# Performance work log

Measured on AMD Instinct MI355X. Metric: run time of the kernel, lower is better.

## Reference

```python
import jax, jax.numpy as jnp
import numpy as np

BATCH, TIMESTEPS, DIM, OUT = 64, 512, 1024, 1024


def setup_inputs() -> dict:
    key = jax.random.key(0)
    k1, k2, k3, k4, k5, k6 = jax.random.split(key, 6)
    # glorot-normal-ish scales for params
    def glorot(k, shape):
        fan_in, fan_out = shape[0], shape[-1]
        std = (2.0 / (fan_in + fan_out)) ** 0.5
        return jax.random.normal(k, shape, dtype=jnp.float32) * std
    return {
        "inputs": jax.random.normal(k1, (BATCH, TIMESTEPS, DIM), dtype=jnp.float32),
        "prev_state": jax.random.normal(k2, (BATCH, OUT), dtype=jnp.float32),
        "Wa": glorot(k3, (OUT, OUT)),
        "Ua": glorot(k4, (DIM, OUT)),
        "Va": glorot(k5, (OUT, 1)),
        "Ba": glorot(k6, (1, OUT)),
    }


def reference(inputs, prev_state, Wa, Ua, Va, Ba):
    # WaS: [B, 1, OUT] broadcast over timesteps
    WaS = jnp.einsum("bo,op->bp", prev_state, Wa)[:, None, :]
    # UaH: [B, T, OUT]
    UaH = jnp.einsum("btd,do->bto", inputs, Ua)
    scores = jnp.tanh(UaH + WaS + Ba)            # [B, T, OUT]
    scores = jax.nn.relu(scores @ Va)            # [B, T, 1]
    sm = jax.nn.softmax(scores, axis=1)          # softmax over timesteps
    context_vector = jnp.sum(inputs * sm, axis=1)  # [B, DIM]
    return context_vector
```

## Files before the change

kernel.cpp:

```cpp
#include <hip/hip_runtime.h>


typedef _Float16 h8 __attribute__((ext_vector_type(8)));
typedef _Float16 h4 __attribute__((ext_vector_type(4)));
typedef float f16v __attribute__((ext_vector_type(16)));

__device__ __forceinline__ float tanh_fast(float x) {
    float e = __expf(2.0f * x);
    return 1.0f - 2.0f * __builtin_amdgcn_rcpf(e + 1.0f);
}

__global__ __launch_bounds__(256) void k_pack_ua(const float* __restrict__ Ua,
                                                 _Float16* __restrict__ B16) {
    int t = blockIdx.x * 256 + threadIdx.x;
    int nn = t & 31, kg = (t >> 5) & 1, ks = (t >> 6) & 63, nt = t >> 12;
    int n = (nt << 5) + nn;
    int kbase = (ks << 4) + (kg << 3);
    h8 v;
#pragma unroll
    for (int j = 0; j < 8; ++j) v[j] = (_Float16)Ua[(size_t)(kbase + j) * 1024 + n];
    *(h8*)(B16 + ((size_t)t << 3)) = v;
}

__global__ __launch_bounds__(256) void k_was_part(const float* __restrict__ ps,
                                                  const float* __restrict__ Wa,
                                                  float* __restrict__ part) {
    int ic = blockIdx.x >> 2, psl = blockIdx.x & 3;
    int tid = threadIdx.x, wv = tid >> 6, lane = tid & 63;
    int p4 = psl * 64 + lane;
    const float4* Wa4 = (const float4*)Wa;
    float4* part4 = (float4*)part;
#pragma unroll 1
    for (int c = 0; c < 4; ++c) {
        int o0 = ic * 128 + c * 32;
        float4 w[32];
#pragma unroll
        for (int o = 0; o < 32; ++o) w[o] = Wa4[(size_t)(o0 + o) * 256 + p4];
#pragma unroll 1
        for (int bb = 0; bb < 16; ++bb) {
            int b = wv * 16 + bb;
            const float* psb = ps + b * 1024 + o0;
            size_t oidx = (size_t)((ic << 6) + b) * 256 + p4;
            float4 a;
            if (c == 0) { a.x = a.y = a.z = a.w = 0.f; }
            else        { a = part4[oidx]; }
#pragma unroll
            for (int o = 0; o < 32; ++o) {
                float s = psb[o];
                a.x += s * w[o].x; a.y += s * w[o].y;
                a.z += s * w[o].z; a.w += s * w[o].w;
            }
            part4[oidx] = a;
        }
    }
}

__global__ __launch_bounds__(256) void k_was_reduce(const float* __restrict__ part,
                                                    const float* __restrict__ Ba,
                                                    float* __restrict__ wsWaS) {
    int b = blockIdx.x, tid = threadIdx.x;
    const float4* p4 = (const float4*)part;
    float4 acc = ((const float4*)Ba)[tid];
#pragma unroll
    for (int ic = 0; ic < 8; ++ic) {
        float4 v = p4[((ic << 6) + b) * 256 + tid];
        acc.x += v.x; acc.y += v.y; acc.z += v.z; acc.w += v.w;
    }
    ((float4*)wsWaS)[b * 256 + tid] = acc;
}

#define AST 136
__global__ __launch_bounds__(256, 1) void k_fused_gemm(
    const float* __restrict__ inputs, const _Float16* __restrict__ B16,
    const float* __restrict__ wsWaS, const float* __restrict__ Va,
    float* __restrict__ scores)
{
    __shared__ _Float16 Ash[2][128 * AST];
    __shared__ float scoreSh[128];
    const int tid = threadIdx.x;
    const int lane = tid & 63, wv = tid >> 6;
    const int l31 = lane & 31, lhi = lane >> 5;
    const int r0 = blockIdx.x * 128;
    const int b = r0 >> 9;
    const int srow = tid >> 1, sq = tid & 1;
    const float4* srcBase = (const float4*)inputs + (size_t)(r0 + srow) * 256 + sq * 16;

    if (tid < 128) scoreSh[tid] = 0.0f;

    for (int pass = 0; pass < 2; ++pass) {
        const int ntb = (pass << 4) + (wv << 2);
        f16v acc[4][4];
#pragma unroll
        for (int rt = 0; rt < 4; ++rt)
#pragma unroll
            for (int ct = 0; ct < 4; ++ct)
#pragma unroll
                for (int e = 0; e < 16; ++e) acc[rt][ct][e] = 0.0f;

        float4 vA[16];
#pragma unroll
        for (int j = 0; j < 16; ++j) vA[j] = srcBase[j];
        {
            _Float16* dst = &Ash[0][srow * AST + sq * 64];
#pragma unroll
            for (int j = 0; j < 8; ++j) {
                float4 v0 = vA[2 * j], v1 = vA[2 * j + 1];
                *(h8*)(dst + j * 8) = (h8){ (_Float16)v0.x, (_Float16)v0.y,
                                            (_Float16)v0.z, (_Float16)v0.w,
                                            (_Float16)v1.x, (_Float16)v1.y,
                                            (_Float16)v1.z, (_Float16)v1.w };
            }
        }
        __syncthreads();

        for (int kc = 0; kc < 8; ++kc) {
            const int buf = kc & 1;
            if (kc < 7) {
                const float4* s2 = srcBase + ((kc + 1) << 5);
#pragma unroll
                for (int j = 0; j < 16; ++j) vA[j] = s2[j];
            }
#pragma unroll
            for (int ks8 = 0; ks8 < 8; ++ks8) {
                const int ks = (kc << 3) + ks8;
                h8 af[4], bf[4];
#pragma unroll
                for (int rt = 0; rt < 4; ++rt)
                    af[rt] = *(const h8*)&Ash[buf][(rt * 32 + l31) * AST + ks8 * 16 + lhi * 8];
#pragma unroll
                for (int ct = 0; ct < 4; ++ct)
                    bf[ct] = *(const h8*)(B16 + ((((ntb + ct) << 6) + ks) << 9) + lane * 8);
#pragma unroll
                for (int rt = 0; rt < 4; ++rt)
#pragma unroll
                    for (int ct = 0; ct < 4; ++ct)
                        acc[rt][ct] = __builtin_amdgcn_mfma_f32_32x32x16_f16(
                            af[rt], bf[ct], acc[rt][ct], 0, 0, 0);
            }
            if (kc < 7) {
                _Float16* dst = &Ash[buf ^ 1][srow * AST + sq * 64];
#pragma unroll
                for (int j = 0; j < 8; ++j) {
                    float4 v0 = vA[2 * j], v1 = vA[2 * j + 1];
                    *(h8*)(dst + j * 8) = (h8){ (_Float16)v0.x, (_Float16)v0.y,
                                                (_Float16)v0.z, (_Float16)v0.w,
                                                (_Float16)v1.x, (_Float16)v1.y,
                                                (_Float16)v1.z, (_Float16)v1.w };
                }
            }
            __syncthreads();
        }
        float wsv[4], vav[4];
#pragma unroll
        for (int ct = 0; ct < 4; ++ct) {
            int n = (pass << 9) + (wv << 7) + (ct << 5) + l31;
            wsv[ct] = wsWaS[b * 1024 + n];
            vav[ct] = Va[n];
        }
#pragma unroll
        for (int rt = 0; rt < 4; ++rt) {
#pragma unroll
            for (int i = 0; i < 16; ++i) {
                float s = 0.0f;
#pragma unroll
                for (int ct = 0; ct < 4; ++ct)
                    s += tanh_fast(acc[rt][ct][i] + wsv[ct]) * vav[ct];
                s += __shfl_xor(s, 1);
                s += __shfl_xor(s, 2);
                s += __shfl_xor(s, 4);
                s += __shfl_xor(s, 8);
                s += __shfl_xor(s, 16);
                if (l31 == 0) {
                    int row = rt * 32 + (i & 3) + ((i >> 2) << 3) + (lhi << 2);
                    atomicAdd(&scoreSh[row], s);
                }
            }
        }
    }
    __syncthreads();
    if (tid < 128) scores[r0 + tid] = fmaxf(scoreSh[tid], 0.0f);
}

__global__ __launch_bounds__(256) void k_softmax(const float* __restrict__ scores,
                                                 float* __restrict__ sm) {
    int b = blockIdx.x, tid = threadIdx.x;
    __shared__ float red[256];
    const float* sb = scores + b * 512;
    float s0 = sb[tid], s1 = sb[tid + 256];
    red[tid] = fmaxf(s0, s1);
    __syncthreads();
    for (int st = 128; st > 0; st >>= 1) {
        if (tid < st) red[tid] = fmaxf(red[tid], red[tid + st]);
        __syncthreads();
    }
    float m = red[0];
    __syncthreads();
    float e0 = __expf(s0 - m), e1 = __expf(s1 - m);
    red[tid] = e0 + e1;
    __syncthreads();
    for (int st = 128; st > 0; st >>= 1) {
        if (tid < st) red[tid] += red[tid + st];
        __syncthreads();
    }
    float inv = 1.0f / red[0];
    sm[b * 512 + tid] = e0 * inv;
    sm[b * 512 + 256 + tid] = e1 * inv;
}

__global__ __launch_bounds__(256) void k_ctx_part(const float* __restrict__ inputs,
                                                  const float* __restrict__ sm,
                                                  float* __restrict__ part) {
    int ts = blockIdx.x, b = blockIdx.y, tid = threadIdx.x;
    const float4* inF4 = (const float4*)inputs;
    float4 acc = {0.f, 0.f, 0.f, 0.f};
    int t0 = ts * 64;
#pragma unroll 8
    for (int t = t0; t < t0 + 64; ++t) {
        float wgt = sm[b * 512 + t];
        float4 x = inF4[(size_t)(b * 512 + t) * 256 + tid];
        acc.x += wgt * x.x; acc.y += wgt * x.y; acc.z += wgt * x.z; acc.w += wgt * x.w;
    }
    ((float4*)part)[((ts << 6) + b) * 256 + tid] = acc;
}

__global__ __launch_bounds__(256) void k_ctx_reduce(const float* __restrict__ part,
                                                    float* __restrict__ out) {
    int g = blockIdx.x * 256 + threadIdx.x;
    const float4* p4 = (const float4*)part;
    float4 acc = p4[g];
#pragma unroll
    for (int s = 1; s < 8; ++s) {
        float4 v = p4[s * 16384 + g];
        acc.x += v.x; acc.y += v.y; acc.z += v.z; acc.w += v.w;
    }
    ((float4*)out)[g] = acc;
}

extern "C" void kernel_launch(void* const* d_in, const int* in_sizes, int n_in,
                              void* d_out, int out_size, void* d_ws, size_t ws_size,
                              hipStream_t stream) {
    const float* inputs = (const float*)d_in[0];
    const float* prev   = (const float*)d_in[1];
    const float* Wa     = (const float*)d_in[2];
    const float* Ua     = (const float*)d_in[3];
    const float* Va     = (const float*)d_in[4];
    const float* Ba     = (const float*)d_in[5];
    float* out = (float*)d_out;

    char* ws = (char*)d_ws;
    _Float16* B16   = (_Float16*)(ws);
    float* wasPart  = (float*)(ws + (2u << 20));
    float* wsWaS    = (float*)(ws + (4u << 20));
    float* scores   = (float*)(ws + (4u << 20) + (256u << 10));
    float* sm       = (float*)(ws + (4u << 20) + (384u << 10));
    float* ctxPart  = (float*)(ws + (4u << 20) + (512u << 10));

    hipLaunchKernelGGL(k_pack_ua,    dim3(512),    dim3(256), 0, stream, Ua, B16);
    hipLaunchKernelGGL(k_was_part,   dim3(32),     dim3(256), 0, stream, prev, Wa, wasPart);
    hipLaunchKernelGGL(k_was_reduce, dim3(64),     dim3(256), 0, stream, wasPart, Ba, wsWaS);
    hipLaunchKernelGGL(k_fused_gemm, dim3(256),    dim3(256), 0, stream, inputs, B16, wsWaS, Va, scores);
    hipLaunchKernelGGL(k_softmax,    dim3(64),     dim3(256), 0, stream, scores, sm);
    hipLaunchKernelGGL(k_ctx_part,   dim3(8, 64),  dim3(256), 0, stream, inputs, sm, ctxPart);
    hipLaunchKernelGGL(k_ctx_reduce, dim3(64),     dim3(256), 0, stream, ctxPart, out);
}
```

Before: 388.3 us.

## Pre-pack inputs to fp16 MFMA layout and stream fragments directly from global

Adds a separate pass that converts the fp32 inputs into an fp16 buffer laid out in MFMA fragment order. The fused GEMM then reads A and B fragments straight from global memory with register double-buffering, with no LDS staging and no barriers. The GEMM tile is halved to 64 rows per block so the grid doubles and two blocks can share a CU. The cost is an extra 64 MB fp16 write plus its read back, and every A fragment is now re-read from global/L2 by all four waves and both passes.

Result: faster. 377.9 us (-2.7%).

```diff
diff --git a/kernel.cpp b/kernel.cpp
--- a/kernel.cpp
+++ b/kernel.cpp
@@ -2,7 +2,6 @@
 
 
 typedef _Float16 h8 __attribute__((ext_vector_type(8)));
-typedef _Float16 h4 __attribute__((ext_vector_type(4)));
 typedef float f16v __attribute__((ext_vector_type(16)));
 
 __device__ __forceinline__ float tanh_fast(float x) {
@@ -20,6 +19,20 @@
 #pragma unroll
     for (int j = 0; j < 8; ++j) v[j] = (_Float16)Ua[(size_t)(kbase + j) * 1024 + n];
     *(h8*)(B16 + ((size_t)t << 3)) = v;
+}
+
+__global__ __launch_bounds__(256) void k_pack_a(const float* __restrict__ inputs,
+                                                _Float16* __restrict__ A16) {
+    int w = blockIdx.x * 4 + (threadIdx.x >> 6);
+    int lane = threadIdx.x & 63;
+    int rb = w >> 6, ks = w & 63;
+    int row = (rb << 5) + (lane & 31);
+    int k = (ks << 4) + ((lane >> 5) << 3);
+    const float4* src = (const float4*)(inputs + ((size_t)row << 10) + k);
+    float4 v0 = src[0], v1 = src[1];
+    h8 o = { (_Float16)v0.x, (_Float16)v0.y, (_Float16)v0.z, (_Float16)v0.w,
+             (_Float16)v1.x, (_Float16)v1.y, (_Float16)v1.z, (_Float16)v1.w };
+    *(h8*)(A16 + (((size_t)w << 6) + lane) * 8) = o;
 }
 
 __global__ __launch_bounds__(256) void k_was_part(const float* __restrict__ ps,
@@ -69,96 +82,71 @@
     ((float4*)wsWaS)[b * 256 + tid] = acc;
 }
 
-#define AST 136
-__global__ __launch_bounds__(256, 1) void k_fused_gemm(
-    const float* __restrict__ inputs, const _Float16* __restrict__ B16,
+__global__ __launch_bounds__(256, 2) void k_fused_gemm(
+    const _Float16* __restrict__ A16, const _Float16* __restrict__ B16,
     const float* __restrict__ wsWaS, const float* __restrict__ Va,
     float* __restrict__ scores)
 {
-    __shared__ _Float16 Ash[2][128 * AST];
-    __shared__ float scoreSh[128];
+    __shared__ float scoreSh[64];
     const int tid = threadIdx.x;
     const int lane = tid & 63, wv = tid >> 6;
     const int l31 = lane & 31, lhi = lane >> 5;
-    const int r0 = blockIdx.x * 128;
+    const int r0 = blockIdx.x * 64;
+    const int rb0 = blockIdx.x * 2;
     const int b = r0 >> 9;
-    const int srow = tid >> 1, sq = tid & 1;
-    const float4* srcBase = (const float4*)inputs + (size_t)(r0 + srow) * 256 + sq * 16;
-
-    if (tid < 128) scoreSh[tid] = 0.0f;
+
+    if (tid < 64) scoreSh[tid] = 0.0f;
+    __syncthreads();
+
+    const h8* A8 = (const h8*)A16;
+    const h8* B8 = (const h8*)B16;
+    const h8* aBase = A8 + ((size_t)rb0 << 12) + lane;
 
     for (int pass = 0; pass < 2; ++pass) {
         const int ntb = (pass << 4) + (wv << 2);
-        f16v acc[4][4];
-#pragma unroll
-        for (int rt = 0; rt < 4; ++rt)
+        const h8* bBase = B8 + ((size_t)ntb << 12) + lane;
+
+        f16v acc[2][4];
+#pragma unroll
+        for (int rt = 0; rt < 2; ++rt)
 #pragma unroll
             for (int ct = 0; ct < 4; ++ct)
 #pragma unroll
                 for (int e = 0; e < 16; ++e) acc[rt][ct][e] = 0.0f;
 
-        float4 vA[16];
-#pragma unroll
-        for (int j = 0; j < 16; ++j) vA[j] = srcBase[j];
-        {
-            _Float16* dst = &Ash[0][srow * AST + sq * 64];
-#pragma unroll
-            for (int j = 0; j < 8; ++j) {
-                float4 v0 = vA[2 * j], v1 = vA[2 * j + 1];
-                *(h8*)(dst + j * 8) = (h8){ (_Float16)v0.x, (_Float16)v0.y,
-                                            (_Float16)v0.z, (_Float16)v0.w,
-                                            (_Float16)v1.x, (_Float16)v1.y,
-                                            (_Float16)v1.z, (_Float16)v1.w };
+        h8 af[2][2], bf[2][4];
+#pragma unroll
+        for (int rt = 0; rt < 2; ++rt) af[0][rt] = aBase[rt * 4096];
+#pragma unroll
+        for (int ct = 0; ct < 4; ++ct) bf[0][ct] = bBase[ct * 4096];
+
+#pragma unroll 4
+        for (int ks = 0; ks < 64; ++ks) {
+            const int cur = ks & 1, nxt = cur ^ 1;
+            if (ks < 63) {
+                const int o = (ks + 1) << 6;
+#pragma unroll
+                for (int rt = 0; rt < 2; ++rt) af[nxt][rt] = aBase[rt * 4096 + o];
+#pragma unroll
+                for (int ct = 0; ct < 4; ++ct) bf[nxt][ct] = bBase[ct * 4096 + o];
             }
-        }
-        __syncthreads();
-
-        for (int kc = 0; kc < 8; ++kc) {
-            const int buf = kc & 1;
-            if (kc < 7) {
-                const float4* s2 = srcBase + ((kc + 1) << 5);
-#pragma unroll
-                for (int j = 0; j < 16; ++j) vA[j] = s2[j];
-            }
-#pragma unroll
-            for (int ks8 = 0; ks8 < 8; ++ks8) {
-                const int ks = (kc << 3) + ks8;
-                h8 af[4], bf[4];
-#pragma unroll
-                for (int rt = 0; rt < 4; ++rt)
-                    af[rt] = *(const h8*)&Ash[buf][(rt * 32 + l31) * AST + ks8 * 16 + lhi * 8];
+#pragma unroll
+            for (int rt = 0; rt < 2; ++rt)
 #pragma unroll
                 for (int ct = 0; ct < 4; ++ct)
-                    bf[ct] = *(const h8*)(B16 + ((((ntb + ct) << 6) + ks) << 9) + lane * 8);
-#pragma unroll
-                for (int rt = 0; rt < 4; ++rt)
-#pragma unroll
-                    for (int ct = 0; ct < 4; ++ct)
-                        acc[rt][ct] = __builtin_amdgcn_mfma_f32_32x32x16_f16(
-                            af[rt], bf[ct], acc[rt][ct], 0, 0, 0);
-            }
-            if (kc < 7) {
-                _Float16* dst = &Ash[buf ^ 1][srow * AST + sq * 64];
-#pragma unroll
-                for (int j = 0; j < 8; ++j) {
-                    float4 v0 = vA[2 * j], v1 = vA[2 * j + 1];
-                    *(h8*)(dst + j * 8) = (h8){ (_Float16)v0.x, (_Float16)v0.y,
-                                                (_Float16)v0.z, (_Float16)v0.w,
-                                                (_Float16)v1.x, (_Float16)v1.y,
-                                                (_Float16)v1.z, (_Float16)v1.w };
-                }
-            }
-            __syncthreads();
-        }
+                    acc[rt][ct] = __builtin_amdgcn_mfma_f32_32x32x16_f16(
+                        af[cur][rt], bf[cur][ct], acc[rt][ct], 0, 0, 0);
+        }
+
         float wsv[4], vav[4];
 #pragma unroll
         for (int ct = 0; ct < 4; ++ct) {
-            int n = (pass << 9) + (wv << 7) + (ct << 5) + l31;
+            int n = (ntb + ct) << 5 | l31;
             wsv[ct] = wsWaS[b * 1024 + n];
             vav[ct] = Va[n];
         }
 #pragma unroll
-        for (int rt = 0; rt < 4; ++rt) {
+        for (int rt = 0; rt < 2; ++rt) {
 #pragma unroll
             for (int i = 0; i < 16; ++i) {
                 float s = 0.0f;
@@ -178,7 +166,7 @@
         }
     }
     __syncthreads();
-    if (tid < 128) scores[r0 + tid] = fmaxf(scoreSh[tid], 0.0f);
+    if (tid < 64) scores[r0 + tid] = fmaxf(scoreSh[tid], 0.0f);
 }
 
 __global__ __launch_bounds__(256) void k_softmax(const float* __restrict__ scores,
@@ -248,17 +236,19 @@
     float* out = (float*)d_out;
 
     char* ws = (char*)d_ws;
-    _Float16* B16   = (_Float16*)(ws);
-    float* wasPart  = (float*)(ws + (2u << 20));
-    float* wsWaS    = (float*)(ws + (4u << 20));
-    float* scores   = (float*)(ws + (4u << 20) + (256u << 10));
-    float* sm       = (float*)(ws + (4u << 20) + (384u << 10));
-    float* ctxPart  = (float*)(ws + (4u << 20) + (512u << 10));
+    _Float16* A16   = (_Float16*)(ws);
+    _Float16* B16   = (_Float16*)(ws + (64u << 20));
+    float* wasPart  = (float*)(ws + (66u << 20));
+    float* wsWaS    = (float*)(ws + (68u << 20));
+    float* scores   = (float*)(ws + (68u << 20) + (256u << 10));
+    float* sm       = (float*)(ws + (68u << 20) + (384u << 10));
+    float* ctxPart  = (float*)(ws + (68u << 20) + (512u << 10));
 
     hipLaunchKernelGGL(k_pack_ua,    dim3(512),    dim3(256), 0, stream, Ua, B16);
+    hipLaunchKernelGGL(k_pack_a,     dim3(16384),  dim3(256), 0, stream, inputs, A16);
     hipLaunchKernelGGL(k_was_part,   dim3(32),     dim3(256), 0, stream, prev, Wa, wasPart);
     hipLaunchKernelGGL(k_was_reduce, dim3(64),     dim3(256), 0, stream, wasPart, Ba, wsWaS);
-    hipLaunchKernelGGL(k_fused_gemm, dim3(256),    dim3(256), 0, stream, inputs, B16, wsWaS, Va, scores);
+    hipLaunchKernelGGL(k_fused_gemm, dim3(512),    dim3(256), 0, stream, A16, B16, wsWaS, Va, scores);
     hipLaunchKernelGGL(k_softmax,    dim3(64),     dim3(256), 0, stream, scores, sm);
     hipLaunchKernelGGL(k_ctx_part,   dim3(8, 64),  dim3(256), 0, stream, inputs, sm, ctxPart);
     hipLaunchKernelGGL(k_ctx_reduce, dim3(64),     dim3(256), 0, stream, ctxPart, out);
```
